# Optimization experiments

Measured on AMD Instinct MI355X. Metric: run time of the kernel, lower is better.

Reference implementation:

```python
import jax, jax.numpy as jnp
import numpy as np
from jax import lax

WHISPER_DIM, WAVLM_DIM, MUQ_DIM = 1280, 1024, 1024
CODEBOOK_SIZE, CODEBOOK_DIM = 8192, 256
B, T_W, T_M = 8, 2048, 1024  # T_w = T_wl = 2048 @50Hz, muq @25Hz -> T_m = 1024
CONCAT_DIM = WHISPER_DIM + WAVLM_DIM + MUQ_DIM


def setup_inputs() -> dict:
    key = jax.random.key(0)
    ks = jax.random.split(key, 10)
    s = 0.02
    return {
        "whisper_feat": jax.random.normal(ks[0], (B, T_W, WHISPER_DIM), jnp.float32),
        "wavlm_feat": jax.random.normal(ks[1], (B, T_W, WAVLM_DIM), jnp.float32),
        "muq_feat": jax.random.normal(ks[2], (B, T_M, MUQ_DIM), jnp.float32),
        # Conv1d weights, torch layout (out_ch, in_ch, k)
        "w_conv_w": jax.random.normal(ks[3], (WHISPER_DIM, WHISPER_DIM, 4), jnp.float32) * s,
        "w_conv_b": jnp.zeros((WHISPER_DIM,), jnp.float32),
        "wl_conv_w": jax.random.normal(ks[4], (WAVLM_DIM, WAVLM_DIM, 4), jnp.float32) * s,
        "wl_conv_b": jnp.zeros((WAVLM_DIM,), jnp.float32),
        # Linear: torch layout (out_features, in_features)
        "proj_w": jax.random.normal(ks[5], (CODEBOOK_DIM, CONCAT_DIM), jnp.float32) * s,
        "proj_b": jnp.zeros((CODEBOOK_DIM,), jnp.float32),
        "codebook": jax.random.normal(ks[6], (CODEBOOK_SIZE, CODEBOOK_DIM), jnp.float32) * 0.02,
    }


def _conv1d_s2(x_btc, w_oik, b):
    # x: (B, T, C) -> (B, C, T) conv k=4 s=2 p=1 -> (B, T//2, C)
    y = lax.conv_general_dilated(
        x_btc.transpose(0, 2, 1), w_oik,
        window_strides=(2,), padding=[(1, 1)],
        dimension_numbers=("NCH", "OIH", "NCH"))
    return (y + b[None, :, None]).transpose(0, 2, 1)


def reference(whisper_feat, wavlm_feat, muq_feat, w_conv_w, w_conv_b,
              wl_conv_w, wl_conv_b, proj_w, proj_b, codebook):
    w = _conv1d_s2(whisper_feat, w_conv_w, w_conv_b)   # (B, 1024, 1280)
    wl = _conv1d_s2(wavlm_feat, wl_conv_w, wl_conv_b)  # (B, 1024, 1024)
    m = muq_feat                                        # (B, 1024, 1024)
    min_len = min(w.shape[1], wl.shape[1], m.shape[1])
    concat = jnp.concatenate([w[:, :min_len], wl[:, :min_len], m[:, :min_len]], axis=-1)
    z_e = jnp.einsum("btc,dc->btd", concat, proj_w) + proj_b  # (B, T, D)

    # VQ: squared-Euclidean argmin against the codebook (same argmin as cdist)
    Bsz, T, D = z_e.shape
    z_flat = z_e.reshape(-1, D)
    d2 = (jnp.sum(z_flat * z_flat, axis=-1, keepdims=True)
          - 2.0 * z_flat @ codebook.T
          + jnp.sum(codebook * codebook, axis=-1)[None, :])  # (B*T, K)
    codes = jnp.argmin(d2, axis=-1)                     # (B*T,)
    z_q = codebook[codes].reshape(Bsz, T, D)
    z_q_st = z_e + lax.stop_gradient(z_q - z_e)
    commit_loss = jnp.mean(jnp.square(z_e - lax.stop_gradient(z_q)))
    return z_q_st, codes.reshape(Bsz, T), commit_loss
```

## Files before the change

### kernel.cpp

```cpp
#include <hip/hip_runtime.h>
#include <cstdint>
#include <cstddef>

typedef unsigned short u16;
typedef __attribute__((ext_vector_type(8))) short bf16x8;
typedef __attribute__((ext_vector_type(4))) float f32x4;
typedef unsigned int u32;
typedef __attribute__((address_space(1))) const u32 gu32;
typedef __attribute__((address_space(3))) u32 lu32;

__device__ __forceinline__ void gload_lds16(const void* g, void* l) {
    __builtin_amdgcn_global_load_lds((gu32*)g, (lu32*)l, 16, 0, 0);
}

__device__ __forceinline__ u16 f2bf(float v) {
    u32 u = __float_as_uint(v);
    return (u16)((u + 0x7fffu + ((u >> 16) & 1u)) >> 16);
}
__device__ __forceinline__ float bf2f(u16 h) { return __uint_as_float(((u32)h) << 16); }

__device__ __forceinline__ void split3(float f, u16& h1, u16& h2, u16& h3) {
    h1 = f2bf(f); float r = f - bf2f(h1);
    h2 = f2bf(r); r -= bf2f(h2);
    h3 = f2bf(r);
}

__device__ __forceinline__ void mfma6(f32x4& c, bf16x8 a1, bf16x8 a2, bf16x8 a3,
                                      bf16x8 b1, bf16x8 b2, bf16x8 b3) {
    c = __builtin_amdgcn_mfma_f32_16x16x32_bf16(a1, b1, c, 0, 0, 0);
    c = __builtin_amdgcn_mfma_f32_16x16x32_bf16(a1, b2, c, 0, 0, 0);
    c = __builtin_amdgcn_mfma_f32_16x16x32_bf16(a2, b1, c, 0, 0, 0);
    c = __builtin_amdgcn_mfma_f32_16x16x32_bf16(a1, b3, c, 0, 0, 0);
    c = __builtin_amdgcn_mfma_f32_16x16x32_bf16(a3, b1, c, 0, 0, 0);
    c = __builtin_amdgcn_mfma_f32_16x16x32_bf16(a2, b2, c, 0, 0, 0);
}

__global__ __launch_bounds__(256)
void split_x8t(const float* __restrict__ x, u16* __restrict__ p0,
               size_t pstr, int I) {
    __shared__ u16 tl[12288];
    const int b = blockIdx.x / 33, blk = blockIdx.x - b * 33;
    const int o0 = blk * 64;
    const int nval = (o0 + 64 <= 2050) ? 64 : (2050 - o0);
    const int c0 = blockIdx.y << 6;
    const int tid = threadIdx.x;
    const int r = tid >> 2, c4 = tid & 3;

    if (r < nval) {
        int local = o0 + r;
        int parity = local >= 1025 ? 1 : 0;
        int idx = local - parity * 1025;
        int prow = 2 * idx + parity;
        bool pad = (prow == 0) || (prow == 2049);
        int s = pad ? 0 : (prow - 1);
        const float* src = x + (size_t)(b * 2048 + s) * I + c0;
#pragma unroll
        for (int k = 0; k < 4; k++) {
            int cf4 = c4 + k * 4;
            float4 v = make_float4(0.f, 0.f, 0.f, 0.f);
            if (!pad) v = *reinterpret_cast<const float4*>(src + cf4 * 4);
            float vals[4] = {v.x, v.y, v.z, v.w};
            int base = ((cf4 >> 1) * 64 + r) * 8 + (cf4 & 1) * 4;
#pragma unroll
            for (int q = 0; q < 4; q++) {
                u16 h1, h2, h3; split3(vals[q], h1, h2, h3);
                tl[base + q]        = h1;
                tl[4096 + base + q] = h2;
                tl[8192 + base + q] = h3;
            }
        }
    }
    __syncthreads();
#pragma unroll
    for (int e = tid; e < 1536; e += 256) {
        int p = e >> 9, rem = e & 511;
        int gs = rem >> 6, rr = rem & 63;
        if (rr < nval) {
            size_t dst = (size_t)p * pstr +
                         (size_t)((c0 >> 3) + gs) * 131200 +
                         (size_t)(b * 2050 + o0 + rr) * 8;
            *reinterpret_cast<bf16x8*>(&p0[dst]) =
                *reinterpret_cast<const bf16x8*>(&tl[p * 4096 + (gs * 64 + rr) * 8]);
        }
    }
}

__global__ __launch_bounds__(256)
void split_rows8t(const float* __restrict__ in, u16* __restrict__ p0,
                  size_t pstr, int R, int C) {
    __shared__ u16 tl[12288];
    const int r0 = blockIdx.x << 6;
    const int c0 = blockIdx.y << 6;
    const int tid = threadIdx.x;
    const int r = tid >> 2, c4 = tid & 3;
    const float* src = in + (size_t)(r0 + r) * C + c0;
#pragma unroll
    for (int k = 0; k < 4; k++) {
        int cf4 = c4 + k * 4;
        float4 v = *reinterpret_cast<const float4*>(src + cf4 * 4);
        float vals[4] = {v.x, v.y, v.z, v.w};
        int base = ((cf4 >> 1) * 64 + r) * 8 + (cf4 & 1) * 4;
#pragma unroll
        for (int q = 0; q < 4; q++) {
            u16 h1, h2, h3; split3(vals[q], h1, h2, h3);
            tl[base + q]        = h1;
            tl[4096 + base + q] = h2;
            tl[8192 + base + q] = h3;
        }
    }
    __syncthreads();
#pragma unroll
    for (int e = tid; e < 1536; e += 256) {
        int p = e >> 9, rem = e & 511;
        int gs = rem >> 6, rr = rem & 63;
        size_t dst = (size_t)p * pstr +
                     ((size_t)((c0 >> 3) + gs) * R + (r0 + rr)) * 8;
        *reinterpret_cast<bf16x8*>(&p0[dst]) =
            *reinterpret_cast<const bf16x8*>(&tl[p * 4096 + (gs * 64 + rr) * 8]);
    }
}

__global__ __launch_bounds__(256)
void split_weightT8m(const float* __restrict__ w, u16* __restrict__ p0,
                     size_t pstr, int I, int O, int NT) {
    __shared__ u16 tl[12288];
    const int o0 = blockIdx.x << 6;
    const int c0 = blockIdx.y << 6;
    const int G = I >> 3;
    const size_t SLAB = (size_t)4 * G * NT * 8;
    const int tid = threadIdx.x;
    const int r = tid >> 2, c4 = tid & 3;
    for (int kcv = 0; kcv < 4; kcv++) {
#pragma unroll
        for (int k = 0; k < 4; k++) {
            int cf4 = c4 + k * 4;
#pragma unroll
            for (int q = 0; q < 4; q++) {
                int i = c0 + cf4 * 4 + q;
                float f = w[((size_t)(o0 + r) * I + i) * 4 + kcv];
                u16 h1, h2, h3; split3(f, h1, h2, h3);
                int base = ((cf4 >> 1) * 64 + r) * 8 + (cf4 & 1) * 4 + q;
                tl[base]        = h1;
                tl[4096 + base] = h2;
                tl[8192 + base] = h3;
            }
        }
        __syncthreads();
        for (int e = tid; e < 1536; e += 256) {
            int p = e >> 9, rem = e & 511;
            int gs = rem >> 6, rr = rem & 63;
            int o = o0 + rr;
            int ng = o / NT, orr = o - ng * NT;
            int kg = kcv * G + (c0 >> 3) + gs;
            size_t dst = (size_t)p * pstr + (size_t)ng * SLAB +
                         (size_t)kg * NT * 8 + (size_t)orr * 8;
            *reinterpret_cast<bf16x8*>(&p0[dst]) =
                *reinterpret_cast<const bf16x8*>(&tl[p * 4096 + (gs * 64 + rr) * 8]);
        }
        __syncthreads();
    }
}

__global__ void cnorm_kernel(const float* __restrict__ cb, float* __restrict__ cn) {
    int w = threadIdx.x >> 6, lane = threadIdx.x & 63;
    int row = blockIdx.x * 4 + w;
    float4 v = *reinterpret_cast<const float4*>(&cb[(size_t)row * 256 + lane * 4]);
    float s = v.x * v.x + v.y * v.y + v.z * v.z + v.w * v.w;
#pragma unroll
    for (int off = 32; off; off >>= 1) s += __shfl_xor(s, off);
    if (lane == 0) cn[row] = s;
}

template<int TN>
__global__ __launch_bounds__(256, 2)
void conv_mfma7(const u16* __restrict__ xs, unsigned pstr_x,
                const u16* __restrict__ wt, unsigned pstr_w,
                const float* __restrict__ bias,
                u16* __restrict__ outp, unsigned pstr_o,
                int I, int O) {
    constexpr int FN = TN / 32;
    constexpr int NB = TN / 16;
    constexpr int BPLANE = 32 * TN;
    constexpr int BUFE = 8192 + 2 * BPLANE;
    __shared__ u16 lds[2 * BUFE];
    const int m0 = blockIdx.x << 7;
    const int ny = blockIdx.y;
    const int n0 = ny * TN;
    const int tid = threadIdx.x, lane = tid & 63, wv = tid >> 6;
    const int wr = ((wv >> 1) & 1) << 6, wc = (wv & 1) * (TN / 2);
    const int fr = lane & 15, fkg = lane >> 4;
    const int b = m0 >> 10, t0 = m0 & 1023;
    const int G = I >> 3;
    const int SL = 131200;
    const int NIT = G, npt = G >> 2;
    const size_t SLAB = (size_t)4 * G * TN * 8;

    const u16* srcp[NB];
    int dsto[NB];
    const int nload = (wv < 2) ? 8 : NB;
    int inc;
    if (wv < 2) {
        inc = 4 * SL;
#pragma unroll
        for (int j = 0; j < NB; j++) {
            if (j < 8) {
                int kg = j >> 1, half = j & 1;
                int r = half * 64 + lane;
                srcp[j] = xs + (size_t)wv * pstr_x + (size_t)kg * SL +
                          (size_t)(b * 2050 + t0 + r) * 8;
                dsto[j] = wv * 4096 + j * 512;
            } else { srcp[j] = xs; dsto[j] = 0; }
        }
    } else {
        inc = BPLANE;
#pragma unroll
        for (int j = 0; j < NB; j++) {
            srcp[j] = wt + (size_t)(wv - 2) * pstr_w + (size_t)ny * SLAB +
                      j * 512 + lane * 8;
            dsto[j] = 8192 + (wv - 2) * BPLANE + j * 512;
        }
    }

    const u16* pa3 = xs + 2 * (size_t)pstr_x + (size_t)fkg * SL +
                     (size_t)(b * 2050 + t0 + wr + fr) * 8;
    const u16* pb3 = wt + 2 * (size_t)pstr_w + (size_t)ny * SLAB +
                     (size_t)fkg * (TN * 8) + (size_t)(wc + fr) * 8;

    f32x4 acc[4][FN];
#pragma unroll
    for (int i = 0; i < 4; i++)
#pragma unroll
        for (int j = 0; j < FN; j++) acc[i][j] = (f32x4){0.f, 0.f, 0.f, 0.f};

#pragma unroll
    for (int j = 0; j < NB; j++)
        if (j < nload) { gload_lds16(srcp[j], &lds[dsto[j]]); srcp[j] += inc; }
    __syncthreads();

    int scnt = npt - 1, skcv = 0;
    int dcnt = npt, dkcv = 0;
    int cur = 0;

    for (int it = 0; it < NIT; ++it) {
        const u16* lb = &lds[cur * BUFE];
        bf16x8 a1[4], a2[4], b1[FN], b2[FN];
#pragma unroll
        for (int fm = 0; fm < 4; fm++) {
            int aidx = fkg * 1024 + (wr + fm * 16 + fr) * 8;
            a1[fm] = *reinterpret_cast<const bf16x8*>(lb + aidx);
            a2[fm] = *reinterpret_cast<const bf16x8*>(lb + 4096 + aidx);
        }
#pragma unroll
        for (int fn = 0; fn < FN; fn++) {
            int bidx = 8192 + fkg * (TN * 8) + (wc + fn * 16 + fr) * 8;
            b1[fn] = *reinterpret_cast<const bf16x8*>(lb + bidx);
            b2[fn] = *reinterpret_cast<const bf16x8*>(lb + BPLANE + bidx);
        }
        if (it + 1 < NIT) {
#pragma unroll
            for (int j = 0; j < NB; j++)
                if (j < nload) {
                    gload_lds16(srcp[j], &lds[(cur ^ 1) * BUFE + dsto[j]]);
                    srcp[j] += inc;
                }
            if (wv < 2) {
                if (--scnt == 0) {
                    int d = ((skcv == 1) ? -8192 : 8200) - (int)pstr_x;
#pragma unroll
                    for (int j = 0; j < 8; j++) srcp[j] += d;
                    skcv++; scnt = npt;
                }
            }
        }
        bf16x8 da3[4], db3[FN];
#pragma unroll
        for (int fm = 0; fm < 4; fm++)
            da3[fm] = *reinterpret_cast<const bf16x8*>(pa3 + fm * 128);
#pragma unroll
        for (int fn = 0; fn < FN; fn++)
            db3[fn] = *reinterpret_cast<const bf16x8*>(pb3 + fn * 128);
        pa3 += 4 * SL;
        pb3 += BPLANE;
        if (--dcnt == 0) {
            pa3 += ((dkcv == 1) ? -8192 : 8200) - (int)pstr_x;
            dkcv++; dcnt = npt;
        }
#pragma unroll
        for (int fm = 0; fm < 4; fm++)
#pragma unroll
            for (int fn = 0; fn < FN; fn++)
                mfma6(acc[fm][fn], a1[fm], a2[fm], da3[fm],
                      b1[fn], b2[fn], db3[fn]);
        __syncthreads();
        cur ^= 1;
    }

    u16 (*eld)[32][TN + 8] = (u16 (*)[32][TN + 8])lds;
    float bv[FN];
#pragma unroll
    for (int fn = 0; fn < FN; fn++) bv[fn] = bias[n0 + wc + fn * 16 + fr];
    const int srb = (wr >> 6) * 16 + fkg * 4;
#pragma unroll
    for (int fm = 0; fm < 4; fm++) {
#pragma unroll
        for (int fn = 0; fn < FN; fn++) {
            int cl = wc + fn * 16 + fr;
#pragma unroll
            for (int j = 0; j < 4; j++) {
                float f = acc[fm][fn][j] + bv[fn];
                u16 h1, h2, h3; split3(f, h1, h2, h3);
                eld[0][srb + j][cl] = h1;
                eld[1][srb + j][cl] = h2;
                eld[2][srb + j][cl] = h3;
            }
        }
        __syncthreads();
        for (int e = tid; e < 96 * (TN / 8); e += 256) {
            int g = e / 96, rem = e - g * 96;
            int p = rem >> 5, sr = rem & 31;
            bf16x8 vv = *reinterpret_cast<const bf16x8*>(&eld[p][sr][g * 8]);
            int rowg = m0 + ((sr >> 4) << 6) + fm * 16 + (sr & 15);
            size_t addr = (size_t)p * pstr_o +
                          (size_t)((n0 >> 3) + g) * 65536 + (size_t)rowg * 8;
            *reinterpret_cast<bf16x8*>(&outp[addr]) = vv;
        }
        __syncthreads();
    }
}

__global__ __launch_bounds__(256, 3)
void proj_mfma5(const u16* __restrict__ sA, const u16* __restrict__ sB,
                const u16* __restrict__ sM, const u16* __restrict__ wp,
                const float* __restrict__ bias, float* __restrict__ z_e,
                u16* __restrict__ zpl) {
    __shared__ u16 lds[24576];
    const int m0 = blockIdx.x << 7;
    const int n0 = blockIdx.y << 7;
    const int tid = threadIdx.x, lane = tid & 63, wv = tid >> 6;
    const int wr = ((wv >> 1) & 1) << 6, wc = (wv & 1) << 6;
    const int fr = lane & 15, fkg = lane >> 4;

    const u16* srcp[12];
    int dsto[12];
#pragma unroll
    for (int j = 0; j < 12; j++) {
        int ii = wv * 12 + j;
        int tile = ii >> 3, sub = ii & 7;
        int kg = sub >> 1, half = sub & 1;
        int r = half * 64 + lane;
        if (tile >= 3)
            srcp[j] = wp + (size_t)(tile - 3) * 851968 + (size_t)kg * 2048 +
                      (size_t)(n0 + r) * 8;
        else
            srcp[j] = nullptr;
        dsto[j] = tile * 4096 + sub * 512;
    }

    f32x4 acc[4][4];
#pragma unroll
    for (int i = 0; i < 4; i++)
#pragma unroll
        for (int j = 0; j < 4; j++) acc[i][j] = (f32x4){0.f, 0.f, 0.f, 0.f};

    const u16* segp[3] = {sA, sB, sM};
    const int segG[3] = {160, 128, 128};
    const unsigned segP[3] = {10485760u, 8388608u, 8388608u};

    for (int seg = 0; seg < 3; seg++) {
        const u16* sp = segp[seg];
        const unsigned sps = segP[seg];
#pragma unroll
        for (int j = 0; j < 12; j++) {
            int ii = wv * 12 + j;
            int tile = ii >> 3, sub = ii & 7;
            int kg = sub >> 1, half = sub & 1;
            int r = half * 64 + lane;
            if (tile < 3)
                srcp[j] = sp + (size_t)tile * sps + (size_t)kg * 65536 +
                          (size_t)(m0 + r) * 8;
        }
        const int niter = segG[seg] >> 2;
        for (int it = 0; it < niter; it++) {
#pragma unroll
            for (int j = 0; j < 12; j++) {
                gload_lds16(srcp[j], &lds[dsto[j]]);
                int ii = wv * 12 + j;
                srcp[j] += (ii >> 3) < 3 ? 262144 : 8192;
            }
            __syncthreads();
            bf16x8 bfr[3][4];
#pragma unroll
            for (int p = 0; p < 3; p++)
#pragma unroll
                for (int fn = 0; fn < 4; fn++)
                    bfr[p][fn] = *reinterpret_cast<const bf16x8*>(
                        &lds[(3 + p) * 4096 + fkg * 1024 + (wc + fn * 16 + fr) * 8]);
#pragma unroll
            for (int fm = 0; fm < 4; fm++) {
                int aidx = fkg * 1024 + (wr + fm * 16 + fr) * 8;
                bf16x8 a1 = *reinterpret_cast<const bf16x8*>(&lds[aidx]);
                bf16x8 a2 = *reinterpret_cast<const bf16x8*>(&lds[4096 + aidx]);
                bf16x8 a3 = *reinterpret_cast<const bf16x8*>(&lds[8192 + aidx]);
#pragma unroll
                for (int fn = 0; fn < 4; fn++)
                    mfma6(acc[fm][fn], a1, a2, a3, bfr[0][fn], bfr[1][fn], bfr[2][fn]);
            }
            __syncthreads();
        }
    }
    u16 (*eld)[32][132] = (u16 (*)[32][132])lds;
    float bv[4];
#pragma unroll
    for (int fn = 0; fn < 4; fn++) bv[fn] = bias[n0 + wc + fn * 16 + fr];
    const int srb = (wr >> 6) * 16 + fkg * 4;
#pragma unroll
    for (int fm = 0; fm < 4; fm++) {
#pragma unroll
        for (int fn = 0; fn < 4; fn++) {
            int cl = wc + fn * 16 + fr;
            int col = n0 + cl;
#pragma unroll
            for (int j = 0; j < 4; j++) {
                float f = acc[fm][fn][j] + bv[fn];
                int rowg = m0 + wr + fm * 16 + fkg * 4 + j;
                z_e[(size_t)rowg * 256 + col] = f;
                u16 h1, h2, h3; split3(f, h1, h2, h3);
                eld[0][srb + j][cl] = h1;
                eld[1][srb + j][cl] = h2;
                eld[2][srb + j][cl] = h3;
            }
        }
        __syncthreads();
#pragma unroll
        for (int q = 0; q < 6; q++) {
            int e = q * 256 + tid;
            int g = e / 96, rem = e - g * 96;
            int p = rem >> 5, sr = rem & 31;
            bf16x8 vv = *reinterpret_cast<const bf16x8*>(&eld[p][sr][g * 8]);
            int rowg = m0 + ((sr >> 4) << 6) + fm * 16 + (sr & 15);
            size_t addr = (size_t)p * 2097152 +
                          (size_t)((n0 >> 3) + g) * 65536 + (size_t)rowg * 8;
            *reinterpret_cast<bf16x8*>(&zpl[addr]) = vv;
        }
        __syncthreads();
    }
}

__global__ __launch_bounds__(256, 3)
void vq_mfma4(const u16* __restrict__ zpl, const u16* __restrict__ cbpl,
              const float* __restrict__ cn, double* __restrict__ pmin,
              int* __restrict__ pidx) {
    __shared__ __align__(16) char smem[49152];
    u16* lds = (u16*)smem;
    const int m0 = blockIdx.x << 7;
    const int n0 = blockIdx.y << 7;
    const int tid = threadIdx.x, lane = tid & 63, wv = tid >> 6;
    const int wr = ((wv >> 1) & 1) << 6, wc = (wv & 1) << 6;
    const int fr = lane & 15, fkg = lane >> 4;

    const u16* srcp[12];
    int dsto[12];
#pragma unroll
    for (int j = 0; j < 12; j++) {
        int ii = wv * 12 + j;
        int tile = ii >> 3, sub = ii & 7;
        int kg = sub >> 1, half = sub & 1;
        int r = half * 64 + lane;
        if (tile < 3)
            srcp[j] = zpl + (size_t)tile * 2097152 + (size_t)kg * 65536 +
                      (size_t)(m0 + r) * 8;
        else
            srcp[j] = cbpl + (size_t)(tile - 3) * 2097152 + (size_t)kg * 65536 +
                      (size_t)(n0 + r) * 8;
        dsto[j] = tile * 4096 + sub * 512;
    }

    f32x4 acc[4][4];
#pragma unroll
    for (int i = 0; i < 4; i++)
#pragma unroll
        for (int j = 0; j < 4; j++) acc[i][j] = (f32x4){0.f, 0.f, 0.f, 0.f};

    for (int kt = 0; kt < 256; kt += 32) {
#pragma unroll
        for (int j = 0; j < 12; j++) {
            gload_lds16(srcp[j], &lds[dsto[j]]);
            srcp[j] += 262144;
        }
        __syncthreads();
        bf16x8 bfr[3][4];
#pragma unroll
        for (int p = 0; p < 3; p++)
#pragma unroll
            for (int fn = 0; fn < 4; fn++)
                bfr[p][fn] = *reinterpret_cast<const bf16x8*>(
                    &lds[(3 + p) * 4096 + fkg * 1024 + (wc + fn * 16 + fr) * 8]);
#pragma unroll
        for (int fm = 0; fm < 4; fm++) {
            int aidx = fkg * 1024 + (wr + fm * 16 + fr) * 8;
            bf16x8 a1 = *reinterpret_cast<const bf16x8*>(&lds[aidx]);
            bf16x8 a2 = *reinterpret_cast<const bf16x8*>(&lds[4096 + aidx]);
            bf16x8 a3 = *reinterpret_cast<const bf16x8*>(&lds[8192 + aidx]);
#pragma unroll
            for (int fn = 0; fn < 4; fn++)
                mfma6(acc[fm][fn], a1, a2, a3, bfr[0][fn], bfr[1][fn], bfr[2][fn]);
        }
        __syncthreads();
    }
    double (*red_d)[32] = (double (*)[32])smem;
    int (*red_n)[32] = (int (*)[32])(smem + 32768);
#pragma unroll
    for (int fm = 0; fm < 4; fm++)
#pragma unroll
        for (int j = 0; j < 4; j++) {
            double best = 1e300; int bestn = 0x7fffffff;
#pragma unroll
            for (int fn = 0; fn < 4; fn++) {
                int gn = n0 + wc + fn * 16 + fr;
                double d = (double)cn[gn] - 2.0 * (double)acc[fm][fn][j];
                if (d < best || (d == best && gn < bestn)) { best = d; bestn = gn; }
            }
            int row = wr + fm * 16 + fkg * 4 + j;
            int cand = ((wv & 1) << 4) + fr;
            red_d[row][cand] = best; red_n[row][cand] = bestn;
        }
    __syncthreads();
    if (tid < 128) {
        double best = red_d[tid][0]; int bestn = red_n[tid][0];
#pragma unroll 4
        for (int k = 1; k < 32; k++) {
            double d = red_d[tid][k]; int n2 = red_n[tid][k];
            if (d < best || (d == best && n2 < bestn)) { best = d; bestn = n2; }
        }
        size_t idx = (size_t)(m0 + tid) * 64 + (n0 >> 7);
        pmin[idx] = best; pidx[idx] = bestn;
    }
}

__global__ void vq_finalize(const double* __restrict__ pmin, const int* __restrict__ pidx,
                            const float* __restrict__ z, const float* __restrict__ cb,
                            float* __restrict__ out, double* __restrict__ cpart) {
    int w = threadIdx.x >> 6, lane = threadIdx.x & 63;
    int m = blockIdx.x * 4 + w;
    double d = pmin[(size_t)m * 64 + lane];
    int n = pidx[(size_t)m * 64 + lane];
#pragma unroll
    for (int off = 32; off; off >>= 1) {
        double d2 = __shfl_xor(d, off);
        int n2 = __shfl_xor(n, off);
        if (d2 < d || (d2 == d && n2 < n)) { d = d2; n = n2; }
    }
    float4 cv = *reinterpret_cast<const float4*>(&cb[(size_t)n * 256 + lane * 4]);
    float4 zv = *reinterpret_cast<const float4*>(&z[(size_t)m * 256 + lane * 4]);
    *reinterpret_cast<float4*>(&out[(size_t)m * 256 + lane * 4]) = cv;
    float dx = zv.x - cv.x, dy = zv.y - cv.y, dz = zv.z - cv.z, dw = zv.w - cv.w;
    double s = (double)(dx * dx) + (double)(dy * dy) + (double)(dz * dz) + (double)(dw * dw);
#pragma unroll
    for (int off = 32; off; off >>= 1) s += __shfl_xor(s, off);
    if (lane == 0) {
        out[2097152 + m] = (float)n;
        cpart[m] = s;
    }
}

__global__ void vq_reduce(const double* __restrict__ cpart, float* __restrict__ out) {
    __shared__ double sm[256];
    double s = 0.0;
    for (int i = threadIdx.x; i < 8192; i += 256) s += cpart[i];
    sm[threadIdx.x] = s;
    __syncthreads();
    for (int off = 128; off; off >>= 1) {
        if ((int)threadIdx.x < off) sm[threadIdx.x] += sm[threadIdx.x + off];
        __syncthreads();
    }
    if (threadIdx.x == 0) out[2105344] = (float)(sm[0] / 2097152.0);
}

extern "C" void kernel_launch(void* const* d_in, const int* in_sizes, int n_in,
                              void* d_out, int out_size, void* d_ws, size_t ws_size,
                              hipStream_t stream) {
    (void)in_sizes; (void)n_in; (void)out_size; (void)ws_size;
    const float* whisper   = (const float*)d_in[0];
    const float* wavlm     = (const float*)d_in[1];
    const float* muq       = (const float*)d_in[2];
    const float* w_conv_w  = (const float*)d_in[3];
    const float* w_conv_b  = (const float*)d_in[4];
    const float* wl_conv_w = (const float*)d_in[5];
    const float* wl_conv_b = (const float*)d_in[6];
    const float* proj_w    = (const float*)d_in[7];
    const float* proj_b    = (const float*)d_in[8];
    const float* codebook  = (const float*)d_in[9];
    float* out = (float*)d_out;
    char* wsb = (char*)d_ws;

    u16*   xsA   = (u16*)(wsb + 0);
    u16*   wtbA  = (u16*)(wsb + 125952000);
    u16*   cApl  = (u16*)(wsb + 176259072);
    u16*   xsB   = (u16*)(wsb + 0);
    u16*   wtbB  = (u16*)(wsb + 100761600);
    u16*   cBpl  = (u16*)(wsb + 125927424);
    u16*   muqpl = (u16*)(wsb + 0);
    u16*   wtpPl = (u16*)(wsb + 50331648);
    float* z_e   = (float*)(wsb + 55443456);
    u16*   zpl   = (u16*)(wsb + 63832064);
    u16*   cbpl  = (u16*)(wsb + 76414976);
    float* cnorm = (float*)(wsb + 88997888);
    double* pmin = (double*)(wsb + 89030656);
    int*    pidx = (int*)(wsb + 93224960);
    double* cpart= (double*)(wsb + 95322112);

    split_x8t<<<dim3(264, 20), 256, 0, stream>>>(whisper, xsA, 20992000, 1280);
    split_weightT8m<<<dim3(20, 20), 256, 0, stream>>>(w_conv_w, wtbA, 6553600,
                                                      1280, 1280, 160);
    conv_mfma7<160><<<dim3(64, 8), 256, 0, stream>>>(xsA, 20992000, wtbA, 6553600,
                                                     w_conv_b, cApl, 10485760,
                                                     1280, 1280);
    split_x8t<<<dim3(264, 16), 256, 0, stream>>>(wavlm, xsB, 16793600, 1024);
    split_weightT8m<<<dim3(16, 16), 256, 0, stream>>>(wl_conv_w, wtbB, 4194304,
                                                      1024, 1024, 128);
    conv_mfma7<128><<<dim3(64, 8), 256, 0, stream>>>(xsB, 16793600, wtbB, 4194304,
                                                     wl_conv_b, cBpl, 8388608,
                                                     1024, 1024);
    split_rows8t<<<dim3(128, 16), 256, 0, stream>>>(muq, muqpl, 8388608, 8192, 1024);
    split_rows8t<<<dim3(4, 52), 256, 0, stream>>>(proj_w, wtpPl, 851968, 256, 3328);
    proj_mfma5<<<dim3(64, 2), 256, 0, stream>>>(cApl, cBpl, muqpl, wtpPl, proj_b, z_e, zpl);
    split_rows8t<<<dim3(128, 4), 256, 0, stream>>>(codebook, cbpl, 2097152, 8192, 256);
    cnorm_kernel<<<2048, 256, 0, stream>>>(codebook, cnorm);
    vq_mfma4<<<dim3(64, 64), 256, 0, stream>>>(zpl, cbpl, cnorm, pmin, pidx);
    vq_finalize<<<2048, 256, 0, stream>>>(pmin, pidx, z_e, codebook, out, cpart);
    vq_reduce<<<1, 256, 0, stream>>>(cpart, out);
}
```

Before: 1.269 ms.

## Double-buffer VQ kernel LDS loads and raise MFMA wave priority

Rewrites the VQ distance kernel so the two high-order bf16 planes are double-buffered in LDS, with the next k-tile's async global-to-LDS loads issued before the current tile's MFMAs. The third (low-order) plane is read straight from global memory into registers, which shrinks the LDS footprint per stage. It also wraps the MFMA blocks in the conv, proj and VQ kernels with s_setprio so that compute-issuing waves get priority. In exchange the VQ kernel uses 64KB of LDS and drops to 2 blocks per CU, and the direct global reads of the third plane may add latency.

```diff
diff --git a/kernel.cpp b/kernel.cpp
--- a/kernel.cpp
+++ b/kernel.cpp
@@ -285,12 +285,14 @@
             pa3 += ((dkcv == 1) ? -8192 : 8200) - (int)pstr_x;
             dkcv++; dcnt = npt;
         }
+        __builtin_amdgcn_s_setprio(1);
 #pragma unroll
         for (int fm = 0; fm < 4; fm++)
 #pragma unroll
             for (int fn = 0; fn < FN; fn++)
                 mfma6(acc[fm][fn], a1[fm], a2[fm], da3[fm],
                       b1[fn], b2[fn], db3[fn]);
+        __builtin_amdgcn_s_setprio(0);
         __syncthreads();
         cur ^= 1;
     }
@@ -395,6 +397,7 @@
                 for (int fn = 0; fn < 4; fn++)
                     bfr[p][fn] = *reinterpret_cast<const bf16x8*>(
                         &lds[(3 + p) * 4096 + fkg * 1024 + (wc + fn * 16 + fr) * 8]);
+            __builtin_amdgcn_s_setprio(1);
 #pragma unroll
             for (int fm = 0; fm < 4; fm++) {
                 int aidx = fkg * 1024 + (wr + fm * 16 + fr) * 8;
@@ -405,6 +408,7 @@
                 for (int fn = 0; fn < 4; fn++)
                     mfma6(acc[fm][fn], a1, a2, a3, bfr[0][fn], bfr[1][fn], bfr[2][fn]);
             }
+            __builtin_amdgcn_s_setprio(0);
             __syncthreads();
         }
     }
@@ -446,11 +450,11 @@
     }
 }
 
-__global__ __launch_bounds__(256, 3)
-void vq_mfma4(const u16* __restrict__ zpl, const u16* __restrict__ cbpl,
+__global__ __launch_bounds__(256, 2)
+void vq_mfma5(const u16* __restrict__ zpl, const u16* __restrict__ cbpl,
               const float* __restrict__ cn, double* __restrict__ pmin,
               int* __restrict__ pidx) {
-    __shared__ __align__(16) char smem[49152];
+    __shared__ __align__(16) char smem[65536];
     u16* lds = (u16*)smem;
     const int m0 = blockIdx.x << 7;
     const int n0 = blockIdx.y << 7;
@@ -458,22 +462,23 @@
     const int wr = ((wv >> 1) & 1) << 6, wc = (wv & 1) << 6;
     const int fr = lane & 15, fkg = lane >> 4;
 
-    const u16* srcp[12];
-    int dsto[12];
-#pragma unroll
-    for (int j = 0; j < 12; j++) {
-        int ii = wv * 12 + j;
-        int tile = ii >> 3, sub = ii & 7;
-        int kg = sub >> 1, half = sub & 1;
-        int r = half * 64 + lane;
-        if (tile < 3)
-            srcp[j] = zpl + (size_t)tile * 2097152 + (size_t)kg * 65536 +
-                      (size_t)(m0 + r) * 8;
-        else
-            srcp[j] = cbpl + (size_t)(tile - 3) * 2097152 + (size_t)kg * 65536 +
-                      (size_t)(n0 + r) * 8;
-        dsto[j] = tile * 4096 + sub * 512;
-    }
+    const u16* srcp[8];
+    int dsto[8];
+    {
+        const u16* bse = (wv < 2) ? (zpl + (size_t)wv * 2097152)
+                                  : (cbpl + (size_t)(wv - 2) * 2097152);
+        int r0 = (wv < 2) ? m0 : n0;
+#pragma unroll
+        for (int j = 0; j < 8; j++) {
+            int kg = j >> 1, half = j & 1;
+            srcp[j] = bse + (size_t)kg * 65536 + (size_t)(r0 + half * 64 + lane) * 8;
+            dsto[j] = wv * 4096 + j * 512;
+        }
+    }
+    const u16* pa3 = zpl + (size_t)2 * 2097152 + (size_t)fkg * 65536 +
+                     (size_t)(m0 + wr + fr) * 8;
+    const u16* pb3 = cbpl + (size_t)2 * 2097152 + (size_t)fkg * 65536 +
+                     (size_t)(n0 + wc + fr) * 8;
 
     f32x4 acc[4][4];
 #pragma unroll
@@ -481,32 +486,57 @@
 #pragma unroll
         for (int j = 0; j < 4; j++) acc[i][j] = (f32x4){0.f, 0.f, 0.f, 0.f};
 
-    for (int kt = 0; kt < 256; kt += 32) {
-#pragma unroll
-        for (int j = 0; j < 12; j++) {
-            gload_lds16(srcp[j], &lds[dsto[j]]);
-            srcp[j] += 262144;
-        }
-        __syncthreads();
-        bf16x8 bfr[3][4];
-#pragma unroll
-        for (int p = 0; p < 3; p++)
-#pragma unroll
-            for (int fn = 0; fn < 4; fn++)
-                bfr[p][fn] = *reinterpret_cast<const bf16x8*>(
-                    &lds[(3 + p) * 4096 + fkg * 1024 + (wc + fn * 16 + fr) * 8]);
+#pragma unroll
+    for (int j = 0; j < 8; j++) {
+        gload_lds16(srcp[j], &lds[dsto[j]]);
+        srcp[j] += 262144;
+    }
+    __syncthreads();
+
+    int cur = 0;
+    for (int it = 0; it < 8; ++it) {
+        const u16* lb = &lds[cur * 16384];
+        bf16x8 a1[4], a2[4], b1[4], b2[4];
 #pragma unroll
         for (int fm = 0; fm < 4; fm++) {
             int aidx = fkg * 1024 + (wr + fm * 16 + fr) * 8;
-            bf16x8 a1 = *reinterpret_cast<const bf16x8*>(&lds[aidx]);
-            bf16x8 a2 = *reinterpret_cast<const bf16x8*>(&lds[4096 + aidx]);
-            bf16x8 a3 = *reinterpret_cast<const bf16x8*>(&lds[8192 + aidx]);
+            a1[fm] = *reinterpret_cast<const bf16x8*>(lb + aidx);
+            a2[fm] = *reinterpret_cast<const bf16x8*>(lb + 4096 + aidx);
+        }
+#pragma unroll
+        for (int fn = 0; fn < 4; fn++) {
+            int bidx = fkg * 1024 + (wc + fn * 16 + fr) * 8;
+            b1[fn] = *reinterpret_cast<const bf16x8*>(lb + 8192 + bidx);
+            b2[fn] = *reinterpret_cast<const bf16x8*>(lb + 12288 + bidx);
+        }
+        if (it + 1 < 8) {
+#pragma unroll
+            for (int j = 0; j < 8; j++) {
+                gload_lds16(srcp[j], &lds[(cur ^ 1) * 16384 + dsto[j]]);
+                srcp[j] += 262144;
+            }
+        }
+        bf16x8 da3[4], db3[4];
+#pragma unroll
+        for (int fm = 0; fm < 4; fm++)
+            da3[fm] = *reinterpret_cast<const bf16x8*>(pa3 + fm * 128);
+#pragma unroll
+        for (int fn = 0; fn < 4; fn++)
+            db3[fn] = *reinterpret_cast<const bf16x8*>(pb3 + fn * 128);
+        pa3 += 262144;
+        pb3 += 262144;
+        __builtin_amdgcn_s_setprio(1);
+#pragma unroll
+        for (int fm = 0; fm < 4; fm++)
 #pragma unroll
             for (int fn = 0; fn < 4; fn++)
-                mfma6(acc[fm][fn], a1, a2, a3, bfr[0][fn], bfr[1][fn], bfr[2][fn]);
-        }
-        __syncthreads();
-    }
+                mfma6(acc[fm][fn], a1[fm], a2[fm], da3[fm],
+                      b1[fn], b2[fn], db3[fn]);
+        __builtin_amdgcn_s_setprio(0);
+        __syncthreads();
+        cur ^= 1;
+    }
+
     double (*red_d)[32] = (double (*)[32])smem;
     int (*red_n)[32] = (int (*)[32])(smem + 32768);
 #pragma unroll
@@ -626,7 +656,7 @@
     proj_mfma5<<<dim3(64, 2), 256, 0, stream>>>(cApl, cBpl, muqpl, wtpPl, proj_b, z_e, zpl);
     split_rows8t<<<dim3(128, 4), 256, 0, stream>>>(codebook, cbpl, 2097152, 8192, 256);
     cnorm_kernel<<<2048, 256, 0, stream>>>(codebook, cnorm);
-    vq_mfma4<<<dim3(64, 64), 256, 0, stream>>>(zpl, cbpl, cnorm, pmin, pidx);
+    vq_mfma5<<<dim3(64, 64), 256, 0, stream>>>(zpl, cbpl, cnorm, pmin, pidx);
     vq_finalize<<<2048, 256, 0, stream>>>(pmin, pidx, z_e, codebook, out, cpart);
     vq_reduce<<<1, 256, 0, stream>>>(cpart, out);
 }
```

After: 1.243 ms. 2.0% less time.
